# Kernel optimization log

Hardware: AMD Instinct MI355X
Metric: run time of the kernel (lower is better)

The kernel has to match this reference:

```python
import jax, jax.numpy as jnp
import numpy as np
import math

N = 50000      # entities per KG
DIM = 128
HEADS = 8
HD = 16        # head dim, HEADS*HD == DIM
L = 2          # GAT layers
E = 800000     # edges per KG
NREL = 2000
T = 200000     # triples per KG (2 columns: pos/neg)
R = 50000      # rules per KG
B = 10000      # alignment seeds
ALPHA = 0.2    # LeakyReLU slope


def _gat_layer(x, src, dst, W, a_s, a_d):
    # x: [N, DIM], W: [DIM, HEADS, HD]
    h = jnp.einsum('nd,dhk->nhk', x, W)                       # [N, H, HD]
    e = jax.nn.leaky_relu(jnp.sum(h * a_s, -1)[src] + jnp.sum(h * a_d, -1)[dst], ALPHA)  # [E, H]
    m = jax.ops.segment_max(e, dst, num_segments=N)           # per-dst max for stable softmax
    m = jnp.where(jnp.isfinite(m), m, 0.0)
    w = jnp.exp(e - m[dst])                                   # [E, H]
    denom = jax.ops.segment_sum(w, dst, num_segments=N)       # [N, H]
    msg = jax.ops.segment_sum(w[:, :, None] * h[src], dst, num_segments=N)  # [N, H, HD]
    return (msg / jnp.maximum(denom, 1e-16)[:, :, None]).reshape(N, HEADS * HD)


def _gat(x, edges, Ws, a_ss, a_ds):
    for l in range(L):
        x = _gat_layer(x, edges[0], edges[1], Ws[l], a_ss[l], a_ds[l])
        if l < L - 1:
            x = jax.nn.elu(x)
    return x


def _l2norm(x):
    return x / jnp.clip(jnp.linalg.norm(x, axis=-1, keepdims=True), 1e-12)


def _truth_value(score):
    return 1.0 - jnp.sum(jnp.abs(score), axis=-1) / (3.0 * math.sqrt(DIM))


def _trans_e(ent, rel, h, t, r):
    return ent[h] + rel[r] - ent[t]


def _rule(ent, rel, rh, rt, rr, prem, tv_col):
    # tv_col: [T, 1]; pad with 1.0 for missing premise
    padded = jnp.concatenate([tv_col, jnp.ones((1, 1), tv_col.dtype)], axis=0)
    rs = _truth_value(_trans_e(ent, rel, rh, rt, rr))          # [R, 1]
    f1 = padded[prem[:, 0]]                                    # [R, 1]
    f2 = padded[prem[:, 1]]
    return 1.0 + f1 * f2 * (rs - 1.0)


def setup_inputs() -> dict:
    key = jax.random.key(0)
    ks = jax.random.split(key, 25)
    ri = lambda k, shape, hi: jax.random.randint(k, shape, 0, hi, dtype=jnp.int64 if jax.config.jax_enable_x64 else jnp.int32)
    return {
        'ent_sr': jax.random.normal(ks[0], (N, DIM), jnp.float32),
        'ent_tg': jax.random.normal(ks[1], (N, DIM), jnp.float32),
        'rel_sr': jax.random.normal(ks[2], (NREL, DIM), jnp.float32),
        'rel_tg': jax.random.normal(ks[3], (NREL, DIM), jnp.float32),
        'gat_W': jax.random.normal(ks[4], (L, DIM, HEADS, HD), jnp.float32) / math.sqrt(DIM),
        'gat_a_src': jax.random.normal(ks[5], (L, HEADS, HD), jnp.float32) / math.sqrt(HD),
        'gat_a_dst': jax.random.normal(ks[6], (L, HEADS, HD), jnp.float32) / math.sqrt(HD),
        'sr_data': ri(ks[7], (B,), N),
        'tg_data': ri(ks[8], (B,), N),
        'edges_sr': ri(ks[9], (2, E), N),
        'edges_tg': ri(ks[10], (2, E), N),
        'h_sr': ri(ks[11], (T, 2), N),
        't_sr': ri(ks[12], (T, 2), N),
        'r_sr': ri(ks[13], (T, 2), NREL),
        'h_tg': ri(ks[14], (T, 2), N),
        't_tg': ri(ks[15], (T, 2), N),
        'r_tg': ri(ks[16], (T, 2), NREL),
        'rh_sr': ri(ks[17], (R, 1), N),
        'rt_sr': ri(ks[18], (R, 1), N),
        'rr_sr': ri(ks[19], (R, 1), NREL),
        'prem_sr': ri(ks[20], (R, 2), T + 1),
        'rh_tg': ri(ks[21], (R, 1), N),
        'rt_tg': ri(ks[22], (R, 1), N),
        'rr_tg': ri(ks[23], (R, 1), NREL),
        'prem_tg': ri(ks[24], (R, 2), T + 1),
    }


def reference(ent_sr, ent_tg, rel_sr, rel_tg, gat_W, gat_a_src, gat_a_dst,
              sr_data, tg_data, edges_sr, edges_tg,
              h_sr, t_sr, r_sr, h_tg, t_tg, r_tg,
              rh_sr, rt_sr, rr_sr, prem_sr, rh_tg, rt_tg, rr_tg, prem_tg):
    g_sr = _gat(ent_sr, edges_sr, gat_W, gat_a_src, gat_a_dst)
    g_tg = _gat(ent_tg, edges_tg, gat_W, gat_a_src, gat_a_dst)
    ng_sr, ng_tg = _l2norm(g_sr), _l2norm(g_tg)
    nrel_sr, nrel_tg = _l2norm(rel_sr), _l2norm(rel_tg)
    sr_tv = _truth_value(_trans_e(ng_sr, nrel_sr, h_sr, t_sr, r_sr))  # [T, 2]
    tg_tv = _truth_value(_trans_e(ng_tg, nrel_tg, h_tg, t_tg, r_tg))  # [T, 2]
    rule_sr = _rule(ng_sr, nrel_sr, rh_sr, rt_sr, rr_sr, prem_sr, sr_tv[:, :1])
    rule_tg = _rule(ng_tg, nrel_tg, rh_tg, rt_tg, rr_tg, prem_tg, tg_tv[:, 1:])
    transe_tv = jnp.concatenate([sr_tv, tg_tv], axis=0)   # [2T, 2]
    rule_tv = jnp.concatenate([rule_sr, rule_tg], axis=0)  # [2R, 1]
    return (g_sr[sr_data], g_tg[tg_data], transe_tv, rule_tv)
```

## Files before the change

### kernel.cpp

```cpp
#include <hip/hip_runtime.h>
#include <hip/hip_bf16.h>

#define N_    50000
#define DIM_  128
#define HEADS_ 8
#define HD_   16
#define E_    800000
#define NREL_ 2000
#define T_    200000
#define R_    50000
#define B_    10000
#define ALPHA_ 0.2f
#define INV3SQRT_ 0.029462782549439484f
#define BSH_  7
#define NB_   391
#define EPB_  2048
#define NBLK_ 391
#define NBLK4_ 392

typedef __attribute__((ext_vector_type(8))) short bf16x8;
typedef __attribute__((ext_vector_type(4))) float f32x4;

__device__ __forceinline__ float bflo(unsigned u) { return __uint_as_float(u << 16); }
__device__ __forceinline__ float bfhi(unsigned u) { return __uint_as_float(u & 0xFFFF0000u); }
__device__ __forceinline__ unsigned pack2bf(float x, float y) {
    __hip_bfloat16 bx = __float2bfloat16(x), by = __float2bfloat16(y);
    unsigned ux = *(unsigned short*)&bx, uy = *(unsigned short*)&by;
    return ux | (uy << 16);
}
__device__ __forceinline__ unsigned short bf1(float x) {
    __hip_bfloat16 b = __float2bfloat16(x);
    return *(unsigned short*)&b;
}

__global__ __launch_bounds__(256) void count_mat_kernel(
        const int* __restrict__ dst0, const int* __restrict__ dst1,
        int* __restrict__ cmat) {
    __shared__ int hist[NB_];
    int blk = blockIdx.x;
    int g = (blk >= NBLK_);
    int bb = g ? blk - NBLK_ : blk;
    const int* dst = g ? dst1 : dst0;
    int t = threadIdx.x;
    for (int i = t; i < NB_; i += 256) hist[i] = 0;
    __syncthreads();
    int e0 = bb * EPB_;
    for (int i = t; i < EPB_; i += 256) {
        int e = e0 + i;
        if (e < E_) atomicAdd(&hist[dst[e] >> BSH_], 1);
    }
    __syncthreads();
    for (int i = t; i < NB_; i += 256)
        cmat[((size_t)(g * NB_ + i)) * NBLK4_ + bb] = hist[i];
}

__global__ __launch_bounds__(256) void rowsum_kernel(const int* __restrict__ cmat, int* __restrict__ tot) {
    int p = blockIdx.x;
    int t = threadIdx.x;
    const int* rowp = cmat + (size_t)p * NBLK4_;
    int s = 0;
    for (int i = t; i < NBLK_; i += 256) s += rowp[i];
#pragma unroll
    for (int m = 1; m < 64; m <<= 1) s += __shfl_xor(s, m);
    __shared__ int ws[4];
    if ((t & 63) == 0) ws[t >> 6] = s;
    __syncthreads();
    if (t == 0) tot[p] = ws[0] + ws[1] + ws[2] + ws[3];
}

__global__ __launch_bounds__(1024) void bucket_scan_kernel(
        const int* __restrict__ tot, int* __restrict__ bbase ,
        int* __restrict__ row_start ) {
    __shared__ int buf[2][512];
    int t = threadIdx.x;
    int g = t >> 9;
    int i = t & 511;
    buf[g][i] = (i < NB_) ? tot[g * NB_ + i] : 0;
    __syncthreads();
#pragma unroll
    for (int off = 1; off < 512; off <<= 1) {
        int v = (i >= off) ? buf[g][i - off] : 0;
        __syncthreads();
        buf[g][i] += v;
        __syncthreads();
    }
    if (i < NB_) bbase[g * (NB_ + 1) + i] = (i == 0) ? 0 : buf[g][i - 1];
    if (i == NB_) {
        bbase[g * (NB_ + 1) + NB_] = buf[g][NB_ - 1];
        row_start[(size_t)g * (N_ + 1) + N_] = buf[g][NB_ - 1];
    }
}

__global__ __launch_bounds__(256) void rowscan_kernel(const int* __restrict__ bbase, int* __restrict__ cmat) {
    __shared__ int ps[256];
    int p = blockIdx.x;
    int t = threadIdx.x;
    int* rowp = cmat + (size_t)p * NBLK4_;
    int a = (2 * t     < NBLK_) ? rowp[2 * t]     : 0;
    int b = (2 * t + 1 < NBLK_) ? rowp[2 * t + 1] : 0;
    ps[t] = a + b;
    __syncthreads();
#pragma unroll
    for (int off = 1; off < 256; off <<= 1) {
        int v = (t >= off) ? ps[t - off] : 0;
        __syncthreads();
        ps[t] += v;
        __syncthreads();
    }
    int g = p / NB_;
    int bk = p - g * NB_;
    int base = bbase[g * (NB_ + 1) + bk];
    int excl = base + ((t > 0) ? ps[t - 1] : 0);
    if (2 * t     < NBLK_) rowp[2 * t]     = excl;
    if (2 * t + 1 < NBLK_) rowp[2 * t + 1] = excl + a;
}

__global__ __launch_bounds__(256) void part_scatter_kernel(
        const int* __restrict__ src0, const int* __restrict__ dst0,
        const int* __restrict__ src1, const int* __restrict__ dst1,
        const int* __restrict__ cmat, int* __restrict__ slab ) {
    __shared__ int lcur[NB_];
    int blk = blockIdx.x;
    int g = (blk >= NBLK_);
    int bb = g ? blk - NBLK_ : blk;
    const int* src = g ? src1 : src0;
    const int* dst = g ? dst1 : dst0;
    int t = threadIdx.x;
    for (int i = t; i < NB_; i += 256)
        lcur[i] = cmat[((size_t)(g * NB_ + i)) * NBLK4_ + bb];
    __syncthreads();
    int e0 = bb * EPB_;
    for (int i = t; i < EPB_; i += 256) {
        int e = e0 + i;
        if (e < E_) {
            int d = dst[e], s = src[e];
            int r = atomicAdd(&lcur[d >> BSH_], 1);
            slab[(size_t)g * E_ + r] = ((d & 127) << 16) | s;
        }
    }
}

__global__ __launch_bounds__(256) void bucket_sort_kernel(
        const int* __restrict__ bbase, const int* __restrict__ slab,
        int* __restrict__ row_start, int* __restrict__ sorted_src) {
    __shared__ int hist[128], pfx[129], cur[128];
    int blk = blockIdx.x;
    int g = (blk >= NB_);
    int bk = g ? blk - NB_ : blk;
    int base = bbase[g * (NB_ + 1) + bk];
    int cnt  = bbase[g * (NB_ + 1) + bk + 1] - base;
    const int* sl = slab + (size_t)g * E_ + base;
    int t = threadIdx.x;
    if (t < 128) hist[t] = 0;
    __syncthreads();
    for (int i = t; i < cnt; i += 256) atomicAdd(&hist[sl[i] >> 16], 1);
    __syncthreads();
    if (t < 128) pfx[t + 1] = hist[t];
    if (t == 0) pfx[0] = 0;
    __syncthreads();
#pragma unroll
    for (int off = 1; off < 128; off <<= 1) {
        int v = (t < 128 && t >= off) ? pfx[t + 1 - off] : 0;
        __syncthreads();
        if (t < 128) pfx[t + 1] += v;
        __syncthreads();
    }
    int node0 = bk << BSH_;
    if (t < 128) {
        int node = node0 + t;
        if (node < N_) row_start[(size_t)g * (N_ + 1) + node] = base + pfx[t];
        cur[t] = 0;
    }
    __syncthreads();
    for (int i = t; i < cnt; i += 256) {
        int v = sl[i];
        int dl = v >> 16;
        int p = pfx[dl] + atomicAdd(&cur[dl], 1);
        sorted_src[(size_t)g * E_ + base + p] = v & 0xFFFF;
    }
}

__global__ __launch_bounds__(256) void prep_wt_kernel(const float* __restrict__ W,
        unsigned short* __restrict__ Wt) {
    int idx = blockIdx.x * 256 + threadIdx.x;
    if (idx >= 2 * 128 * 128) return;
    int l = idx >> 14;
    int rem = idx & 16383;
    int o = rem >> 7, k = rem & 127;
    Wt[idx] = bf1(W[l * 16384 + k * 128 + o]);
}

__global__ __launch_bounds__(256) void gemm_mfma_both_kernel(
        const void* __restrict__ xsrc0, const void* __restrict__ xsrc1, int src_f32,
        const unsigned short* __restrict__ Wt ,
        unsigned short* __restrict__ hout , int half_grid) {
    __shared__ unsigned short xs[32][136];
    int blk = blockIdx.x;
    int g = (blk >= half_grid);
    int bb = g ? blk - half_grid : blk;
    int nbase = bb * 32;
    int t = threadIdx.x;
    {
        int row = t >> 3, c0 = (t & 7) * 16;
        int node = nbase + row;
        if (node >= N_) node = N_ - 1;
        if (src_f32) {
            const float* x = (const float*)(g ? xsrc1 : xsrc0);
            const float4* xr = (const float4*)&x[(size_t)node * 128 + c0];
            float4 v0 = xr[0], v1 = xr[1], v2 = xr[2], v3 = xr[3];
            unsigned* dstp = (unsigned*)&xs[row][c0];
            dstp[0] = pack2bf(v0.x, v0.y); dstp[1] = pack2bf(v0.z, v0.w);
            dstp[2] = pack2bf(v1.x, v1.y); dstp[3] = pack2bf(v1.z, v1.w);
            dstp[4] = pack2bf(v2.x, v2.y); dstp[5] = pack2bf(v2.z, v2.w);
            dstp[6] = pack2bf(v3.x, v3.y); dstp[7] = pack2bf(v3.z, v3.w);
        } else {
            const unsigned short* x = (const unsigned short*)(g ? xsrc1 : xsrc0);
            uint4 v0 = *(const uint4*)&x[(size_t)node * 128 + c0];
            uint4 v1 = *(const uint4*)&x[(size_t)node * 128 + c0 + 8];
            *(uint4*)&xs[row][c0] = v0;
            *(uint4*)&xs[row][c0 + 8] = v1;
        }
    }
    __syncthreads();
    int wave = t >> 6, lane = t & 63;
    int n0 = wave * 32;
    int lr = lane & 15, lk = (lane >> 4) * 8;
    f32x4 acc00 = {0.f,0.f,0.f,0.f}, acc01 = {0.f,0.f,0.f,0.f};
    f32x4 acc10 = {0.f,0.f,0.f,0.f}, acc11 = {0.f,0.f,0.f,0.f};
#pragma unroll
    for (int ks = 0; ks < 128; ks += 32) {
        uint4 ra0 = *(const uint4*)&xs[lr][ks + lk];
        uint4 ra1 = *(const uint4*)&xs[16 + lr][ks + lk];
        uint4 rb0 = *(const uint4*)&Wt[(size_t)(n0 + lr) * 128 + ks + lk];
        uint4 rb1 = *(const uint4*)&Wt[(size_t)(n0 + 16 + lr) * 128 + ks + lk];
        bf16x8 a0 = *(bf16x8*)&ra0, a1 = *(bf16x8*)&ra1;
        bf16x8 b0 = *(bf16x8*)&rb0, b1 = *(bf16x8*)&rb1;
        acc00 = __builtin_amdgcn_mfma_f32_16x16x32_bf16(a0, b0, acc00, 0, 0, 0);
        acc01 = __builtin_amdgcn_mfma_f32_16x16x32_bf16(a0, b1, acc01, 0, 0, 0);
        acc10 = __builtin_amdgcn_mfma_f32_16x16x32_bf16(a1, b0, acc10, 0, 0, 0);
        acc11 = __builtin_amdgcn_mfma_f32_16x16x32_bf16(a1, b1, acc11, 0, 0, 0);
    }
    unsigned short* ho = hout + (size_t)g * N_ * 128;
    int rbase = (lane >> 4) * 4;
#pragma unroll
    for (int r = 0; r < 4; r++) {
        int n0r = nbase + rbase + r;
        int n1r = nbase + 16 + rbase + r;
        if (n0r < N_) {
            ho[(size_t)n0r * 128 + n0 + lr]      = bf1(acc00[r]);
            ho[(size_t)n0r * 128 + n0 + 16 + lr] = bf1(acc01[r]);
        }
        if (n1r < N_) {
            ho[(size_t)n1r * 128 + n0 + lr]      = bf1(acc10[r]);
            ho[(size_t)n1r * 128 + n0 + 16 + lr] = bf1(acc11[r]);
        }
    }
}

__global__ __launch_bounds__(256) void alpha_both_kernel(
        const unsigned short* __restrict__ hb ,
        const float* __restrict__ avs, const float* __restrict__ avd,
        float* __restrict__ asrc, float* __restrict__ adst) {
    int wave = threadIdx.x >> 6, lane = threadIdx.x & 63;
    int idx = blockIdx.x * 4 + wave;
    if (idx >= 2 * N_) return;
    int g = (idx >= N_);
    int node = g ? idx - N_ : idx;
    const unsigned* hrow = (const unsigned*)(hb + (size_t)g * N_ * 128 + (size_t)node * 128);
    unsigned hv = hrow[lane];
    float h0 = bflo(hv), h1 = bfhi(hv);
    float2 s = *(const float2*)&avs[lane * 2];
    float2 d = *(const float2*)&avd[lane * 2];
    float ps = h0 * s.x + h1 * s.y;
    float pd = h0 * d.x + h1 * d.y;
#pragma unroll
    for (int m = 1; m < 8; m <<= 1) {
        ps += __shfl_xor(ps, m);
        pd += __shfl_xor(pd, m);
    }
    if ((lane & 7) == 0) {
        int head = lane >> 3;
        asrc[(size_t)g * N_ * HEADS_ + node * HEADS_ + head] = ps;
        adst[(size_t)g * N_ * HEADS_ + node * HEADS_ + head] = pd;
    }
}

__global__ __launch_bounds__(256) void gat_aggregate_both_kernel(
        const unsigned short* __restrict__ hb ,
        const float* __restrict__ asrc, const float* __restrict__ adst,
        const int* __restrict__ row_start, const int* __restrict__ sorted_src,
        void* __restrict__ out0, void* __restrict__ out1, int apply_elu, int out_bf16) {
    int wave = threadIdx.x >> 6;
    int lane = threadIdx.x & 63;
    int idx = blockIdx.x * 4 + wave;
    if (idx >= 2 * N_) return;
    int g = (idx >= N_);
    int node = g ? idx - N_ : idx;
    const unsigned short* hbt = hb + (size_t)g * N_ * 128;
    const float* as = asrc + (size_t)g * N_ * HEADS_;
    const float* adp = adst + (size_t)g * N_ * HEADS_;
    const int* rs = row_start + (size_t)g * (N_ + 1);
    const int* ss = sorted_src + (size_t)g * E_;

    int e8 = lane >> 3;
    int head = lane & 7;
    float ad = adp[node * HEADS_ + head];
    int beg = rs[node], end = rs[node + 1];
    float denom = 0.f;
    float acc[16];
#pragma unroll
    for (int k = 0; k < 16; k++) acc[k] = 0.f;
    int iters = (end - beg + 7) >> 3;
    for (int k = 0; k < iters; k++) {
        int i = beg + k * 8 + e8;
        if (i < end) {
            int s = ss[i];
            float e = as[s * HEADS_ + head] + ad;
            e = (e >= 0.f) ? e : ALPHA_ * e;
            const uint4* hp = (const uint4*)&hbt[(size_t)s * 128 + head * 16];
            uint4 A = hp[0], Bv = hp[1];
            float w = __expf(e);
            denom += w;
            acc[0]  += w * bflo(A.x);  acc[1]  += w * bfhi(A.x);
            acc[2]  += w * bflo(A.y);  acc[3]  += w * bfhi(A.y);
            acc[4]  += w * bflo(A.z);  acc[5]  += w * bfhi(A.z);
            acc[6]  += w * bflo(A.w);  acc[7]  += w * bfhi(A.w);
            acc[8]  += w * bflo(Bv.x); acc[9]  += w * bfhi(Bv.x);
            acc[10] += w * bflo(Bv.y); acc[11] += w * bfhi(Bv.y);
            acc[12] += w * bflo(Bv.z); acc[13] += w * bfhi(Bv.z);
            acc[14] += w * bflo(Bv.w); acc[15] += w * bfhi(Bv.w);
        }
    }
#pragma unroll
    for (int off = 8; off < 64; off <<= 1) {
        denom += __shfl_xor(denom, off);
#pragma unroll
        for (int k2 = 0; k2 < 16; k2++)
            acc[k2] += __shfl_xor(acc[k2], off);
    }
    float invd = 1.0f / fmaxf(denom, 1e-16f);
    float v0 = acc[e8 * 2] * invd;
    float v1 = acc[e8 * 2 + 1] * invd;
    if (apply_elu) {
        v0 = (v0 > 0.f) ? v0 : (__expf(v0) - 1.f);
        v1 = (v1 > 0.f) ? v1 : (__expf(v1) - 1.f);
    }
    if (out_bf16) {
        unsigned* ob = (unsigned*)(g ? out1 : out0);
        ob[(size_t)node * 64 + head * 8 + e8] = pack2bf(v0, v1);
    } else {
        float* of = (float*)(g ? out1 : out0);
        *(float2*)&of[(size_t)node * DIM_ + head * HD_ + e8 * 2] = make_float2(v0, v1);
    }
}

__global__ __launch_bounds__(256) void normpack_all_kernel(
        const float* __restrict__ g_sr, const float* __restrict__ g_tg,
        const float* __restrict__ rel_sr, const float* __restrict__ rel_tg,
        unsigned* __restrict__ ng_sr, unsigned* __restrict__ ng_tg,
        unsigned* __restrict__ nrel_sr, unsigned* __restrict__ nrel_tg) {
    int row = blockIdx.x * 4 + (threadIdx.x >> 6);
    int lane = threadIdx.x & 63;
    const float* v; unsigned* o; int r;
    if (row < N_)                 { v = g_sr;   o = ng_sr;   r = row; }
    else if (row < 2 * N_)        { v = g_tg;   o = ng_tg;   r = row - N_; }
    else if (row < 2 * N_ + NREL_){ v = rel_sr; o = nrel_sr; r = row - 2 * N_; }
    else if (row < 2 * (N_ + NREL_)) { v = rel_tg; o = nrel_tg; r = row - 2 * N_ - NREL_; }
    else return;
    float2 a = *(const float2*)&v[(size_t)r * DIM_ + lane * 2];
    float s = a.x * a.x + a.y * a.y;
#pragma unroll
    for (int m = 1; m < 64; m <<= 1) s += __shfl_xor(s, m);
    float inv = 1.0f / fmaxf(sqrtf(s), 1e-12f);
    o[(size_t)r * 64 + lane] = pack2bf(a.x * inv, a.y * inv);
}

__global__ __launch_bounds__(256) void transe_both_kernel(
        const unsigned* __restrict__ ng0, const unsigned* __restrict__ nr0,
        const int* __restrict__ h0, const int* __restrict__ t0, const int* __restrict__ r0,
        const unsigned* __restrict__ ng1, const unsigned* __restrict__ nr1,
        const int* __restrict__ h1, const int* __restrict__ t1, const int* __restrict__ r1,
        float* __restrict__ out_tv) {
    int gt = blockIdx.x * 256 + threadIdx.x;
    int item = gt >> 4;
    int l16 = threadIdx.x & 15;
    if (item >= 4 * T_) return;
    const unsigned *ng, *nr;
    const int *hi, *ti, *ri;
    int k;
    if (item < 2 * T_) { ng = ng0; nr = nr0; hi = h0; ti = t0; ri = r0; k = item; }
    else               { ng = ng1; nr = nr1; hi = h1; ti = t1; ri = r1; k = item - 2 * T_; }
    int hh = hi[k], tt = ti[k], rr = ri[k];
    const uint4* ph = (const uint4*)&ng[(size_t)hh * 64 + l16 * 4];
    const uint4* pt = (const uint4*)&ng[(size_t)tt * 64 + l16 * 4];
    const uint4* pr = (const uint4*)&nr[(size_t)rr * 64 + l16 * 4];
    uint4 H = ph[0], Tt = pt[0], Rr = pr[0];
    float s = 0.f;
    s += fabsf(bflo(H.x) + bflo(Rr.x) - bflo(Tt.x));
    s += fabsf(bfhi(H.x) + bfhi(Rr.x) - bfhi(Tt.x));
    s += fabsf(bflo(H.y) + bflo(Rr.y) - bflo(Tt.y));
    s += fabsf(bfhi(H.y) + bfhi(Rr.y) - bfhi(Tt.y));
    s += fabsf(bflo(H.z) + bflo(Rr.z) - bflo(Tt.z));
    s += fabsf(bfhi(H.z) + bfhi(Rr.z) - bfhi(Tt.z));
    s += fabsf(bflo(H.w) + bflo(Rr.w) - bflo(Tt.w));
    s += fabsf(bfhi(H.w) + bfhi(Rr.w) - bfhi(Tt.w));
#pragma unroll
    for (int m = 1; m < 16; m <<= 1) s += __shfl_xor(s, m);
    if (l16 == 0) out_tv[item] = 1.0f - s * INV3SQRT_;
}

__global__ __launch_bounds__(256) void rule_both_kernel(
        const unsigned* __restrict__ ng0, const unsigned* __restrict__ nr0,
        const int* __restrict__ rh0, const int* __restrict__ rt0, const int* __restrict__ rr0,
        const int* __restrict__ prem0, const float* __restrict__ tvcol0,
        const unsigned* __restrict__ ng1, const unsigned* __restrict__ nr1,
        const int* __restrict__ rh1, const int* __restrict__ rt1, const int* __restrict__ rr1,
        const int* __restrict__ prem1, const float* __restrict__ tvcol1,
        float* __restrict__ out_rule) {
    int gt = blockIdx.x * 256 + threadIdx.x;
    int item = gt >> 4;
    int l16 = threadIdx.x & 15;
    if (item >= 2 * R_) return;
    const unsigned *ng, *nr;
    const int *rh, *rt, *rr, *prem;
    const float* tvcol;
    int k;
    if (item < R_) { ng = ng0; nr = nr0; rh = rh0; rt = rt0; rr = rr0; prem = prem0; tvcol = tvcol0; k = item; }
    else           { ng = ng1; nr = nr1; rh = rh1; rt = rt1; rr = rr1; prem = prem1; tvcol = tvcol1; k = item - R_; }
    int hh = rh[k], tt = rt[k], rx = rr[k];
    const uint4* ph = (const uint4*)&ng[(size_t)hh * 64 + l16 * 4];
    const uint4* pt = (const uint4*)&ng[(size_t)tt * 64 + l16 * 4];
    const uint4* pr = (const uint4*)&nr[(size_t)rx * 64 + l16 * 4];
    uint4 H = ph[0], Tt = pt[0], Rr = pr[0];
    float s = 0.f;
    s += fabsf(bflo(H.x) + bflo(Rr.x) - bflo(Tt.x));
    s += fabsf(bfhi(H.x) + bfhi(Rr.x) - bfhi(Tt.x));
    s += fabsf(bflo(H.y) + bflo(Rr.y) - bflo(Tt.y));
    s += fabsf(bfhi(H.y) + bfhi(Rr.y) - bfhi(Tt.y));
    s += fabsf(bflo(H.z) + bflo(Rr.z) - bflo(Tt.z));
    s += fabsf(bfhi(H.z) + bfhi(Rr.z) - bfhi(Tt.z));
    s += fabsf(bflo(H.w) + bflo(Rr.w) - bflo(Tt.w));
    s += fabsf(bfhi(H.w) + bfhi(Rr.w) - bfhi(Tt.w));
#pragma unroll
    for (int m = 1; m < 16; m <<= 1) s += __shfl_xor(s, m);
    if (l16 == 0) {
        float rs = 1.0f - s * INV3SQRT_;
        int p0 = prem[k * 2], p1 = prem[k * 2 + 1];
        float f1 = (p0 < T_) ? tvcol[(size_t)p0 * 2] : 1.0f;
        float f2 = (p1 < T_) ? tvcol[(size_t)p1 * 2] : 1.0f;
        out_rule[item] = 1.0f + f1 * f2 * (rs - 1.0f);
    }
}

__global__ __launch_bounds__(256) void gather_both_kernel(
        const float* __restrict__ g0, const int* __restrict__ data0,
        const float* __restrict__ g1, const int* __restrict__ data1,
        float* __restrict__ out) {
    int i = blockIdx.x * 256 + threadIdx.x;
    if (i >= 2 * B_ * DIM_) return;
    const float* g = (i < B_ * DIM_) ? g0 : g1;
    const int* data = (i < B_ * DIM_) ? data0 : data1;
    int j = (i < B_ * DIM_) ? i : i - B_ * DIM_;
    int r = j >> 7, o = j & 127;
    out[i] = g[(size_t)data[r] * DIM_ + o];
}


extern "C" void kernel_launch(void* const* d_in, const int* in_sizes, int n_in,
                              void* d_out, int out_size, void* d_ws, size_t ws_size,
                              hipStream_t stream) {
    const float* ent_sr = (const float*)d_in[0];
    const float* ent_tg = (const float*)d_in[1];
    const float* rel_sr = (const float*)d_in[2];
    const float* rel_tg = (const float*)d_in[3];
    const float* gat_W  = (const float*)d_in[4];
    const float* a_src  = (const float*)d_in[5];
    const float* a_dst  = (const float*)d_in[6];
    const int* sr_data  = (const int*)d_in[7];
    const int* tg_data  = (const int*)d_in[8];
    const int* edges_sr = (const int*)d_in[9];
    const int* edges_tg = (const int*)d_in[10];
    const int* h_sr = (const int*)d_in[11];
    const int* t_sr = (const int*)d_in[12];
    const int* r_sr = (const int*)d_in[13];
    const int* h_tg = (const int*)d_in[14];
    const int* t_tg = (const int*)d_in[15];
    const int* r_tg = (const int*)d_in[16];
    const int* rh_sr = (const int*)d_in[17];
    const int* rt_sr = (const int*)d_in[18];
    const int* rr_sr = (const int*)d_in[19];
    const int* prem_sr = (const int*)d_in[20];
    const int* rh_tg = (const int*)d_in[21];
    const int* rt_tg = (const int*)d_in[22];
    const int* rr_tg = (const int*)d_in[23];
    const int* prem_tg = (const int*)d_in[24];

    float* out = (float*)d_out;

    size_t off = 0;
    auto alloc = [&](size_t bytes) {
        void* p = (char*)d_ws + off;
        off += (bytes + 255) & ~(size_t)255;
        return p;
    };
    float* g_sr   = (float*)alloc((size_t)N_ * DIM_ * 4);
    float* g_tg   = (float*)alloc((size_t)N_ * DIM_ * 4);
    unsigned short* hb_buf = (unsigned short*)alloc((size_t)2 * N_ * 128 * 2);
    unsigned* x2b = (unsigned*)alloc((size_t)2 * N_ * 64 * 4);
    float* asrc_b = (float*)alloc((size_t)2 * N_ * HEADS_ * 4);
    float* adst_b = (float*)alloc((size_t)2 * N_ * HEADS_ * 4);
    unsigned* ng_sr = (unsigned*)alloc((size_t)N_ * 64 * 4);
    unsigned* ng_tg = (unsigned*)alloc((size_t)N_ * 64 * 4);
    unsigned* nrel_sr = (unsigned*)alloc((size_t)NREL_ * 64 * 4);
    unsigned* nrel_tg = (unsigned*)alloc((size_t)NREL_ * 64 * 4);
    int* sorted_src = (int*)alloc((size_t)2 * E_ * 4);
    int* row_start  = (int*)alloc((size_t)2 * (N_ + 1) * 4);
    int* slab       = (int*)alloc((size_t)2 * E_ * 4);
    int* cmat       = (int*)alloc((size_t)2 * NB_ * NBLK4_ * 4);
    int* tot        = (int*)alloc((size_t)2 * NB_ * 4);
    int* bbase      = (int*)alloc((size_t)2 * (NB_ + 1) * 4);
    unsigned short* Wt = (unsigned short*)alloc((size_t)2 * 128 * 128 * 2);

    const float* as0 = a_src;        const float* as1 = a_src + HEADS_ * HD_;
    const float* ad0 = a_dst;        const float* ad1 = a_dst + HEADS_ * HD_;

    const size_t OFF_G_TG  = (size_t)B_ * DIM_;
    const size_t OFF_TV    = (size_t)2 * B_ * DIM_;
    const size_t OFF_RULE  = OFF_TV + (size_t)4 * T_;

    const int GEMM_GRID = (N_ + 31) / 32;
    const int AGG_GRID  = (2 * N_ + 3) / 4;

    const int* esrc_sr = edges_sr;          const int* edst_sr = edges_sr + E_;
    const int* esrc_tg = edges_tg;          const int* edst_tg = edges_tg + E_;
    unsigned* x2b_sr = x2b;                 unsigned* x2b_tg = x2b + (size_t)N_ * 64;

    prep_wt_kernel<<<(2 * 128 * 128 + 255) / 256, 256, 0, stream>>>(gat_W, Wt);

    count_mat_kernel<<<2 * NBLK_, 256, 0, stream>>>(edst_sr, edst_tg, cmat);
    rowsum_kernel<<<2 * NB_, 256, 0, stream>>>(cmat, tot);
    bucket_scan_kernel<<<1, 1024, 0, stream>>>(tot, bbase, row_start);
    rowscan_kernel<<<2 * NB_, 256, 0, stream>>>(bbase, cmat);
    part_scatter_kernel<<<2 * NBLK_, 256, 0, stream>>>(
        esrc_sr, edst_sr, esrc_tg, edst_tg, cmat, slab);
    bucket_sort_kernel<<<2 * NB_, 256, 0, stream>>>(bbase, slab, row_start, sorted_src);

    gemm_mfma_both_kernel<<<2 * GEMM_GRID, 256, 0, stream>>>(
        ent_sr, ent_tg, 1, Wt, hb_buf, GEMM_GRID);
    alpha_both_kernel<<<AGG_GRID, 256, 0, stream>>>(hb_buf, as0, ad0, asrc_b, adst_b);
    gat_aggregate_both_kernel<<<AGG_GRID, 256, 0, stream>>>(
        hb_buf, asrc_b, adst_b, row_start, sorted_src, x2b_sr, x2b_tg, 1, 1);
    gemm_mfma_both_kernel<<<2 * GEMM_GRID, 256, 0, stream>>>(
        x2b_sr, x2b_tg, 0, Wt + 128 * 128, hb_buf, GEMM_GRID);
    alpha_both_kernel<<<AGG_GRID, 256, 0, stream>>>(hb_buf, as1, ad1, asrc_b, adst_b);
    gat_aggregate_both_kernel<<<AGG_GRID, 256, 0, stream>>>(
        hb_buf, asrc_b, adst_b, row_start, sorted_src, g_sr, g_tg, 0, 0);

    normpack_all_kernel<<<(2 * (N_ + NREL_) + 3) / 4, 256, 0, stream>>>(
        g_sr, g_tg, rel_sr, rel_tg, ng_sr, ng_tg, nrel_sr, nrel_tg);

    transe_both_kernel<<<(4 * T_ * 16 + 255) / 256, 256, 0, stream>>>(
        ng_sr, nrel_sr, h_sr, t_sr, r_sr,
        ng_tg, nrel_tg, h_tg, t_tg, r_tg,
        out + OFF_TV);

    rule_both_kernel<<<(2 * R_ * 16 + 255) / 256, 256, 0, stream>>>(
        ng_sr, nrel_sr, rh_sr, rt_sr, rr_sr, prem_sr, out + OFF_TV + 0,
        ng_tg, nrel_tg, rh_tg, rt_tg, rr_tg, prem_tg, out + OFF_TV + (size_t)2 * T_ + 1,
        out + OFF_RULE);

    gather_both_kernel<<<(2 * B_ * DIM_ + 255) / 256, 256, 0, stream>>>(
        g_sr, sr_data, g_tg, tg_data, out);
}
```

Baseline: 352.2 us.

## Fuse attention-logit computation into GEMM and L2 norm into final aggregate

Attention source and destination logits are now computed in the MFMA GEMM epilogue from the fp32 accumulators, so the separate alpha kernel is gone and the h buffer is not re-read. The final-layer aggregate kernel also computes the row L2 norm and writes the normalized bf16 embedding directly, so the entity normpack pass over g_sr and g_tg is removed and only relation rows are still normalized separately. This saves two kernel launches and one full read of the node features, at the cost of extra shuffle reductions in the GEMM epilogue. The logits now come from fp32 accumulators rather than the bf16-rounded h, which slightly changes numerics.

```diff
diff --git a/kernel.cpp b/kernel.cpp
--- a/kernel.cpp
+++ b/kernel.cpp
@@ -193,7 +193,9 @@
 __global__ __launch_bounds__(256) void gemm_mfma_both_kernel(
         const void* __restrict__ xsrc0, const void* __restrict__ xsrc1, int src_f32,
         const unsigned short* __restrict__ Wt ,
-        unsigned short* __restrict__ hout , int half_grid) {
+        const float* __restrict__ avs, const float* __restrict__ avd,
+        unsigned short* __restrict__ hout ,
+        float* __restrict__ asrc, float* __restrict__ adst, int half_grid) {
     __shared__ unsigned short xs[32][136];
     int blk = blockIdx.x;
     int g = (blk >= half_grid);
@@ -255,33 +257,36 @@
             ho[(size_t)n1r * 128 + n0 + 16 + lr] = bf1(acc11[r]);
         }
     }
-}
-
-__global__ __launch_bounds__(256) void alpha_both_kernel(
-        const unsigned short* __restrict__ hb ,
-        const float* __restrict__ avs, const float* __restrict__ avd,
-        float* __restrict__ asrc, float* __restrict__ adst) {
-    int wave = threadIdx.x >> 6, lane = threadIdx.x & 63;
-    int idx = blockIdx.x * 4 + wave;
-    if (idx >= 2 * N_) return;
-    int g = (idx >= N_);
-    int node = g ? idx - N_ : idx;
-    const unsigned* hrow = (const unsigned*)(hb + (size_t)g * N_ * 128 + (size_t)node * 128);
-    unsigned hv = hrow[lane];
-    float h0 = bflo(hv), h1 = bfhi(hv);
-    float2 s = *(const float2*)&avs[lane * 2];
-    float2 d = *(const float2*)&avd[lane * 2];
-    float ps = h0 * s.x + h1 * s.y;
-    float pd = h0 * d.x + h1 * d.y;
-#pragma unroll
-    for (int m = 1; m < 8; m <<= 1) {
-        ps += __shfl_xor(ps, m);
-        pd += __shfl_xor(pd, m);
-    }
-    if ((lane & 7) == 0) {
-        int head = lane >> 3;
-        asrc[(size_t)g * N_ * HEADS_ + node * HEADS_ + head] = ps;
-        adst[(size_t)g * N_ * HEADS_ + node * HEADS_ + head] = pd;
+    float as_lo = avs[n0 + lr], as_hi = avs[n0 + 16 + lr];
+    float ad_lo = avd[n0 + lr], ad_hi = avd[n0 + 16 + lr];
+    float* asp = asrc + (size_t)g * N_ * HEADS_;
+    float* adp = adst + (size_t)g * N_ * HEADS_;
+    int h0i = 2 * wave, h1i = 2 * wave + 1;
+#pragma unroll
+    for (int r = 0; r < 4; r++) {
+        float ps0 = acc00[r] * as_lo, ps1 = acc01[r] * as_hi;
+        float pd0 = acc00[r] * ad_lo, pd1 = acc01[r] * ad_hi;
+        float qs0 = acc10[r] * as_lo, qs1 = acc11[r] * as_hi;
+        float qd0 = acc10[r] * ad_lo, qd1 = acc11[r] * ad_hi;
+#pragma unroll
+        for (int mm = 1; mm < 16; mm <<= 1) {
+            ps0 += __shfl_xor(ps0, mm); ps1 += __shfl_xor(ps1, mm);
+            pd0 += __shfl_xor(pd0, mm); pd1 += __shfl_xor(pd1, mm);
+            qs0 += __shfl_xor(qs0, mm); qs1 += __shfl_xor(qs1, mm);
+            qd0 += __shfl_xor(qd0, mm); qd1 += __shfl_xor(qd1, mm);
+        }
+        if (lr == 0) {
+            int n0r = nbase + rbase + r;
+            int n1r = nbase + 16 + rbase + r;
+            if (n0r < N_) {
+                asp[n0r * HEADS_ + h0i] = ps0; asp[n0r * HEADS_ + h1i] = ps1;
+                adp[n0r * HEADS_ + h0i] = pd0; adp[n0r * HEADS_ + h1i] = pd1;
+            }
+            if (n1r < N_) {
+                asp[n1r * HEADS_ + h0i] = qs0; asp[n1r * HEADS_ + h1i] = qs1;
+                adp[n1r * HEADS_ + h0i] = qd0; adp[n1r * HEADS_ + h1i] = qd1;
+            }
+        }
     }
 }
 
@@ -289,7 +294,9 @@
         const unsigned short* __restrict__ hb ,
         const float* __restrict__ asrc, const float* __restrict__ adst,
         const int* __restrict__ row_start, const int* __restrict__ sorted_src,
-        void* __restrict__ out0, void* __restrict__ out1, int apply_elu, int out_bf16) {
+        void* __restrict__ out0, void* __restrict__ out1,
+        unsigned* __restrict__ ng0, unsigned* __restrict__ ng1,
+        int apply_elu, int out_bf16) {
     int wave = threadIdx.x >> 6;
     int lane = threadIdx.x & 63;
     int idx = blockIdx.x * 4 + wave;
@@ -349,23 +356,25 @@
         unsigned* ob = (unsigned*)(g ? out1 : out0);
         ob[(size_t)node * 64 + head * 8 + e8] = pack2bf(v0, v1);
     } else {
+        float ssum = v0 * v0 + v1 * v1;
+#pragma unroll
+        for (int off = 1; off < 64; off <<= 1) ssum += __shfl_xor(ssum, off);
+        float inv = 1.0f / fmaxf(sqrtf(ssum), 1e-12f);
         float* of = (float*)(g ? out1 : out0);
         *(float2*)&of[(size_t)node * DIM_ + head * HD_ + e8 * 2] = make_float2(v0, v1);
-    }
-}
-
-__global__ __launch_bounds__(256) void normpack_all_kernel(
-        const float* __restrict__ g_sr, const float* __restrict__ g_tg,
+        unsigned* ngp = g ? ng1 : ng0;
+        ngp[(size_t)node * 64 + head * 8 + e8] = pack2bf(v0 * inv, v1 * inv);
+    }
+}
+
+__global__ __launch_bounds__(256) void normpack_rel_kernel(
         const float* __restrict__ rel_sr, const float* __restrict__ rel_tg,
-        unsigned* __restrict__ ng_sr, unsigned* __restrict__ ng_tg,
         unsigned* __restrict__ nrel_sr, unsigned* __restrict__ nrel_tg) {
     int row = blockIdx.x * 4 + (threadIdx.x >> 6);
     int lane = threadIdx.x & 63;
     const float* v; unsigned* o; int r;
-    if (row < N_)                 { v = g_sr;   o = ng_sr;   r = row; }
-    else if (row < 2 * N_)        { v = g_tg;   o = ng_tg;   r = row - N_; }
-    else if (row < 2 * N_ + NREL_){ v = rel_sr; o = nrel_sr; r = row - 2 * N_; }
-    else if (row < 2 * (N_ + NREL_)) { v = rel_tg; o = nrel_tg; r = row - 2 * N_ - NREL_; }
+    if (row < NREL_)          { v = rel_sr; o = nrel_sr; r = row; }
+    else if (row < 2 * NREL_) { v = rel_tg; o = nrel_tg; r = row - NREL_; }
     else return;
     float2 a = *(const float2*)&v[(size_t)r * DIM_ + lane * 2];
     float s = a.x * a.x + a.y * a.y;
@@ -546,18 +555,18 @@
     bucket_sort_kernel<<<2 * NB_, 256, 0, stream>>>(bbase, slab, row_start, sorted_src);
 
     gemm_mfma_both_kernel<<<2 * GEMM_GRID, 256, 0, stream>>>(
-        ent_sr, ent_tg, 1, Wt, hb_buf, GEMM_GRID);
-    alpha_both_kernel<<<AGG_GRID, 256, 0, stream>>>(hb_buf, as0, ad0, asrc_b, adst_b);
+        ent_sr, ent_tg, 1, Wt, as0, ad0, hb_buf, asrc_b, adst_b, GEMM_GRID);
     gat_aggregate_both_kernel<<<AGG_GRID, 256, 0, stream>>>(
-        hb_buf, asrc_b, adst_b, row_start, sorted_src, x2b_sr, x2b_tg, 1, 1);
+        hb_buf, asrc_b, adst_b, row_start, sorted_src, x2b_sr, x2b_tg,
+        (unsigned*)nullptr, (unsigned*)nullptr, 1, 1);
     gemm_mfma_both_kernel<<<2 * GEMM_GRID, 256, 0, stream>>>(
-        x2b_sr, x2b_tg, 0, Wt + 128 * 128, hb_buf, GEMM_GRID);
-    alpha_both_kernel<<<AGG_GRID, 256, 0, stream>>>(hb_buf, as1, ad1, asrc_b, adst_b);
+        x2b_sr, x2b_tg, 0, Wt + 128 * 128, as1, ad1, hb_buf, asrc_b, adst_b, GEMM_GRID);
     gat_aggregate_both_kernel<<<AGG_GRID, 256, 0, stream>>>(
-        hb_buf, asrc_b, adst_b, row_start, sorted_src, g_sr, g_tg, 0, 0);
-
-    normpack_all_kernel<<<(2 * (N_ + NREL_) + 3) / 4, 256, 0, stream>>>(
-        g_sr, g_tg, rel_sr, rel_tg, ng_sr, ng_tg, nrel_sr, nrel_tg);
+        hb_buf, asrc_b, adst_b, row_start, sorted_src, g_sr, g_tg,
+        ng_sr, ng_tg, 0, 0);
+
+    normpack_rel_kernel<<<(2 * NREL_ + 3) / 4, 256, 0, stream>>>(
+        rel_sr, rel_tg, nrel_sr, nrel_tg);
 
     transe_both_kernel<<<(4 * T_ * 16 + 255) / 256, 256, 0, stream>>>(
         ng_sr, nrel_sr, h_sr, t_sr, r_sr,
```

Result: faster. 337.1 us (-4.3%).
